# Kernel optimization log

Hardware: AMD Instinct MI355X
Metric: run time of the kernel (lower is better)

The kernel has to match this reference:

```python
import jax, jax.numpy as jnp
import numpy as np

SEQ_LEN = 4096
D_IN = 1024
D_OUT = 1024


def setup_inputs() -> dict:
    key = jax.random.key(0)
    k_x, k_q, k_k, k_v = jax.random.split(key, 4)
    s = 1.0 / np.sqrt(D_IN)
    return {
        "x": jax.random.normal(k_x, (SEQ_LEN, D_IN), dtype=jnp.float32),
        "W_query": jax.random.normal(k_q, (D_IN, D_OUT), dtype=jnp.float32) * s,
        "W_key": jax.random.normal(k_k, (D_IN, D_OUT), dtype=jnp.float32) * s,
        "W_value": jax.random.normal(k_v, (D_IN, D_OUT), dtype=jnp.float32) * s,
    }


def reference(x, W_query, W_key, W_value):
    # QKV projections (Linear without bias): [S, d_out]
    q = x @ W_query
    k = x @ W_key
    v = x @ W_value
    # Full S x S score matrix, causal mask, scaled softmax
    scores = q @ k.T  # [S, S]
    seq_len = x.shape[0]
    causal = jnp.tril(jnp.ones((seq_len, seq_len), dtype=bool))
    scores = jnp.where(causal, scores, -jnp.inf)
    scale = 1.0 / jnp.sqrt(jnp.asarray(k.shape[-1], dtype=scores.dtype))
    attn = jax.nn.softmax(scores * scale, axis=-1)
    return attn @ v  # [S, d_out]
```

## Files before the change

### kernel.cpp

```cpp
#include <hip/hip_runtime.h>
#include <math.h>

#define SEQ 4096
#define DIM 1024

typedef unsigned short u16;
typedef __attribute__((ext_vector_type(8))) short short8;
typedef __attribute__((ext_vector_type(4))) float floatx4;
typedef __attribute__((ext_vector_type(4))) unsigned short us4;

__device__ __forceinline__ float bf2f(u16 u) {
    union { unsigned int i; float f; } c; c.i = ((unsigned int)u) << 16; return c.f;
}
__device__ __forceinline__ u16 f2bf(float f) {
    union { float f; unsigned int i; } c; c.f = f;
    return (u16)((c.i + 0x7fffu + ((c.i >> 16) & 1u)) >> 16);
}
__device__ __forceinline__ void gload_lds16(const u16* g, u16* l) {
    __builtin_amdgcn_global_load_lds((const __attribute__((address_space(1))) void*)g,
                                     (__attribute__((address_space(3))) void*)l, 16, 0, 0);
}

template <int MODE>
__global__ __launch_bounds__(256) void gemm_nt(const u16* __restrict__ A,
                                               const u16* __restrict__ B,
                                               void* __restrict__ Cv,
                                               u16* __restrict__ VtOut,
                                               float* __restrict__ Lsum,
                                               int lda, int ldb, int ldc, int Kdim,
                                               float scale0) {
    int row0, col0, kbeg = 0, kend = Kdim;
    if (MODE == 1) {
        const int t = blockIdx.x;
        int by = (int)((sqrtf(8.0f * t + 1.0f) - 1.0f) * 0.5f);
        while ((by + 1) * (by + 2) / 2 <= t) ++by;
        while (by * (by + 1) / 2 > t) --by;
        const int bx = t - by * (by + 1) / 2;
        row0 = by * 128;
        col0 = bx * 128;
    } else if (MODE == 2) {
        col0 = blockIdx.x * 128;
        const int u = blockIdx.y;
        int r;
        if (u < 16) { r = 16 + u; kbeg = 0; kend = 2048; }
        else {
            r = 47 - u;
            kend = r * 128 + 128;
            kbeg = (u < 32) ? 2048 : 0;
        }
        row0 = r * 128;
    } else {
        row0 = blockIdx.y * 128;
        col0 = blockIdx.x * 128;
    }

    __shared__ u16 As[3][4096];
    __shared__ u16 Bs[3][4096];

    const int tid  = threadIdx.x;
    const int wave = tid >> 6;
    const int lane = tid & 63;
    const int wm = wave & 1;
    const int wn = wave >> 1;

    const int s0 = wave * 128 + lane;
    const int s1 = s0 + 64;
    const int r0s = s0 >> 2, q0s = ((s0 & 3) ^ ((s0 >> 3) & 3)) * 8;
    const int r1s = s1 >> 2, q1s = ((s1 & 3) ^ ((s1 >> 3) & 3)) * 8;
    const u16* aP0 = A + (size_t)(row0 + r0s) * lda + kbeg + q0s;
    const u16* aP1 = A + (size_t)(row0 + r1s) * lda + kbeg + q1s;
    const u16* bP0 = B + (size_t)(col0 + r0s) * ldb + kbeg + q0s;
    const u16* bP1 = B + (size_t)(col0 + r1s) * ldb + kbeg + q1s;
    const int l0 = wave * 1024;

    floatx4 acc[4][4] = {};
    const int niter = (kend - kbeg) >> 5;
    const int frow = lane & 15;
    const int xq = (((lane >> 4) ^ ((frow >> 1) & 3))) * 8;

    gload_lds16(aP0, &As[0][l0]);
    gload_lds16(aP1, &As[0][l0 + 512]);
    gload_lds16(bP0, &Bs[0][l0]);
    gload_lds16(bP1, &Bs[0][l0 + 512]);
    aP0 += 32; aP1 += 32; bP0 += 32; bP1 += 32;
    gload_lds16(aP0, &As[1][l0]);
    gload_lds16(aP1, &As[1][l0 + 512]);
    gload_lds16(bP0, &Bs[1][l0]);
    gload_lds16(bP1, &Bs[1][l0 + 512]);
    aP0 += 32; aP1 += 32; bP0 += 32; bP1 += 32;

    auto compute_tile = [&](int c) {
        short8 af[4], bfr[4];
#pragma unroll
        for (int t = 0; t < 4; ++t) {
            af[t]  = *(const short8*)&As[c][(wm * 64 + t * 16 + frow) * 32 + xq];
            bfr[t] = *(const short8*)&Bs[c][(wn * 64 + t * 16 + frow) * 32 + xq];
        }
#pragma unroll
        for (int mt = 0; mt < 4; ++mt)
#pragma unroll
            for (int nt = 0; nt < 4; ++nt)
                acc[mt][nt] = __builtin_amdgcn_mfma_f32_16x16x32_bf16(
                    af[mt], bfr[nt], acc[mt][nt], 0, 0, 0);
    };

    int cur = 0, pre = 2;
    for (int it = 0; it < niter - 2; ++it) {
        asm volatile("s_waitcnt vmcnt(4)\n\ts_barrier" ::: "memory");
        short8 af[4], bfr[4];
#pragma unroll
        for (int t = 0; t < 4; ++t) {
            af[t]  = *(const short8*)&As[cur][(wm * 64 + t * 16 + frow) * 32 + xq];
            bfr[t] = *(const short8*)&Bs[cur][(wn * 64 + t * 16 + frow) * 32 + xq];
        }
        gload_lds16(aP0, &As[pre][l0]);
        gload_lds16(aP1, &As[pre][l0 + 512]);
        gload_lds16(bP0, &Bs[pre][l0]);
        gload_lds16(bP1, &Bs[pre][l0 + 512]);
        aP0 += 32; aP1 += 32; bP0 += 32; bP1 += 32;
#pragma unroll
        for (int mt = 0; mt < 4; ++mt)
#pragma unroll
            for (int nt = 0; nt < 4; ++nt)
                acc[mt][nt] = __builtin_amdgcn_mfma_f32_16x16x32_bf16(
                    af[mt], bfr[nt], acc[mt][nt], 0, 0, 0);
        cur = (cur == 2) ? 0 : cur + 1;
        pre = (pre == 2) ? 0 : pre + 1;
    }
    asm volatile("s_waitcnt vmcnt(4)\n\ts_barrier" ::: "memory");
    compute_tile(cur);
    cur = (cur == 2) ? 0 : cur + 1;
    asm volatile("s_waitcnt vmcnt(0)\n\ts_barrier" ::: "memory");
    compute_tile(cur);

    const int cr = (lane >> 4) * 4;
    const int cc = lane & 15;
    if (MODE == 1) {
        u16* dst = (u16*)Cv;
#pragma unroll
        for (int mt = 0; mt < 4; ++mt) {
#pragma unroll
            for (int r = 0; r < 4; ++r) {
                const int grow = row0 + wm * 64 + mt * 16 + cr + r;
                float rowsum = 0.f;
#pragma unroll
                for (int nt = 0; nt < 4; ++nt) {
                    const int gcol = col0 + wn * 64 + nt * 16 + cc;
                    const float e = (gcol <= grow) ? __expf(acc[mt][nt][r]) : 0.f;
                    rowsum += e;
                    dst[(size_t)grow * ldc + gcol] = f2bf(e);
                }
                rowsum += __shfl_xor(rowsum, 1);
                rowsum += __shfl_xor(rowsum, 2);
                rowsum += __shfl_xor(rowsum, 4);
                rowsum += __shfl_xor(rowsum, 8);
                if (cc == 0) atomicAdd(&Lsum[grow], rowsum);
            }
        }
    } else if (MODE == 2) {
        float* O = (float*)Cv;
        const bool direct = (kbeg == 0) && (kend == row0 + 128);
#pragma unroll
        for (int mt = 0; mt < 4; ++mt)
#pragma unroll
            for (int r = 0; r < 4; ++r) {
                const int grow = row0 + wm * 64 + mt * 16 + cr + r;
                const float invl = __builtin_amdgcn_rcpf(Lsum[grow]);
#pragma unroll
                for (int nt = 0; nt < 4; ++nt) {
                    const int col = col0 + wn * 64 + nt * 16 + cc;
                    const float v = acc[mt][nt][r] * invl;
                    if (direct)
                        O[(size_t)grow * ldc + col] = v;
                    else
                        atomicAdd(&O[(size_t)grow * ldc + col], v);
                }
            }
    } else if (MODE == 0 && col0 >= 2048) {
#pragma unroll
        for (int mt = 0; mt < 4; ++mt)
#pragma unroll
            for (int nt = 0; nt < 4; ++nt) {
                const int row = row0 + wm * 64 + mt * 16 + cr;
                const int col = (col0 - 2048) + wn * 64 + nt * 16 + cc;
                us4 o = { f2bf(acc[mt][nt][0]), f2bf(acc[mt][nt][1]),
                          f2bf(acc[mt][nt][2]), f2bf(acc[mt][nt][3]) };
                *(us4*)&VtOut[(size_t)col * SEQ + row] = o;
            }
    } else {
        u16* dst = (u16*)Cv;
        const float sc = (col0 < 1024) ? scale0 : 1.0f;
#pragma unroll
        for (int mt = 0; mt < 4; ++mt)
#pragma unroll
            for (int nt = 0; nt < 4; ++nt)
#pragma unroll
                for (int r = 0; r < 4; ++r) {
                    const int row = row0 + wm * 64 + mt * 16 + cr + r;
                    const int col = col0 + wn * 64 + nt * 16 + cc;
                    dst[(size_t)row * ldc + col] = f2bf(acc[mt][nt][r] * sc);
                }
    }
}

__global__ __launch_bounds__(256) void prep(const float* __restrict__ x,
                                            const float* __restrict__ W0,
                                            const float* __restrict__ W1,
                                            const float* __restrict__ W2,
                                            u16* __restrict__ xb,
                                            u16* __restrict__ Wt,
                                            float* __restrict__ O,
                                            float* __restrict__ Lsum) {
    __shared__ float tile[32][33];
    const int b = blockIdx.x;
    const int tid = threadIdx.x;
    if (b < 4096) {
        const size_t i = ((size_t)b * 256 + tid) * 4;
        const float4 v = *(const float4*)(x + i);
        us4 o = { f2bf(v.x), f2bf(v.y), f2bf(v.z), f2bf(v.w) };
        *(us4*)(xb + i) = o;
    } else if (b < 7168) {
        const int t = b - 4096;
        const int z = t >> 10;
        const int idx = t & 1023;
        const float* W = (z == 0) ? W0 : (z == 1) ? W1 : W2;
        u16* out = Wt + (size_t)z * DIM * DIM;
        const int bx = (idx & 31) * 32;
        const int by = (idx >> 5) * 32;
        const int tx = tid & 31;
        const int ty = (tid >> 5) * 4;
#pragma unroll
        for (int r = 0; r < 4; ++r)
            tile[ty + r][tx] = W[(size_t)(by + ty + r) * DIM + bx + tx];
        __syncthreads();
#pragma unroll
        for (int r = 0; r < 4; ++r)
            out[(size_t)(bx + ty + r) * DIM + by + tx] = f2bf(tile[tx][ty + r]);
    } else {
        const int t = b - 7168;
        const size_t i = (size_t)2048 * DIM + ((size_t)t * 256 + tid) * 4;
        *(float4*)(O + i) = make_float4(0.f, 0.f, 0.f, 0.f);
        if (t < 4) *(float4*)(Lsum + (size_t)(t * 256 + tid) * 4) =
            make_float4(0.f, 0.f, 0.f, 0.f);
    }
}

extern "C" void kernel_launch(void* const* d_in, const int* in_sizes, int n_in,
                              void* d_out, int out_size, void* d_ws, size_t ws_size,
                              hipStream_t stream) {
    const float* x  = (const float*)d_in[0];
    const float* Wq = (const float*)d_in[1];
    const float* Wk = (const float*)d_in[2];
    const float* Wv = (const float*)d_in[3];

    u16* xb    = (u16*)d_ws;
    u16* Wt    = xb  + (size_t)SEQ * DIM;
    u16* QK    = Wt  + (size_t)3072 * DIM;
    u16* Vt    = QK  + (size_t)SEQ * 2048;
    u16* E     = Vt  + (size_t)DIM * SEQ;
    float* Lsum = (float*)(E + (size_t)SEQ * SEQ);

    prep<<<7680, 256, 0, stream>>>(x, Wq, Wk, Wv, xb, Wt, (float*)d_out, Lsum);

    gemm_nt<0><<<dim3(24, 32), 256, 0, stream>>>(
        xb, Wt, QK, Vt, nullptr, DIM, DIM, 2048, DIM, 0.03125f);

    gemm_nt<1><<<528, 256, 0, stream>>>(
        QK, QK + 1024, E, nullptr, Lsum, 2048, 2048, SEQ, DIM, 1.0f);

    gemm_nt<2><<<dim3(8, 48), 256, 0, stream>>>(
        E, Vt, d_out, nullptr, Lsum, SEQ, SEQ, DIM, SEQ, 1.0f);
}
```

Before: 191.5 us.

## Use 64-row tiles in PV GEMM with paired scheduling, drop split-K atomics

The attention-times-V GEMM now uses 64x128 output tiles over 512 blocks, pairing short and long causal rows by interleaving, so each block covers its full K range. This replaces the earlier 128-row tiling with split-K and float atomicAdd, and removes the zero-initialisation of the output in the prep kernel. The cost is lower MFMA reuse per block (2x4 instead of 4x4 tiles) and more B-tile reloads, and the longest blocks now walk all 4096 K columns alone.

```diff
diff --git a/kernel.cpp b/kernel.cpp
--- a/kernel.cpp
+++ b/kernel.cpp
@@ -40,21 +40,17 @@
         col0 = bx * 128;
     } else if (MODE == 2) {
         col0 = blockIdx.x * 128;
-        const int u = blockIdx.y;
-        int r;
-        if (u < 16) { r = 16 + u; kbeg = 0; kend = 2048; }
-        else {
-            r = 47 - u;
-            kend = r * 128 + 128;
-            kbeg = (u < 32) ? 2048 : 0;
-        }
-        row0 = r * 128;
+        const int y = blockIdx.y;
+        const int r = (y < 32) ? (y << 1) : (63 - ((y - 32) << 1));
+        row0 = r * 64;
+        kbeg = 0;
+        kend = row0 + 64;
     } else {
         row0 = blockIdx.y * 128;
         col0 = blockIdx.x * 128;
     }
 
-    __shared__ u16 As[3][4096];
+    __shared__ u16 As[3][(MODE == 2) ? 2048 : 4096];
     __shared__ u16 Bs[3][4096];
 
     const int tid  = threadIdx.x;
@@ -63,41 +59,50 @@
     const int wm = wave & 1;
     const int wn = wave >> 1;
 
-    const int s0 = wave * 128 + lane;
-    const int s1 = s0 + 64;
-    const int r0s = s0 >> 2, q0s = ((s0 & 3) ^ ((s0 >> 3) & 3)) * 8;
-    const int r1s = s1 >> 2, q1s = ((s1 & 3) ^ ((s1 >> 3) & 3)) * 8;
-    const u16* aP0 = A + (size_t)(row0 + r0s) * lda + kbeg + q0s;
-    const u16* aP1 = A + (size_t)(row0 + r1s) * lda + kbeg + q1s;
-    const u16* bP0 = B + (size_t)(col0 + r0s) * ldb + kbeg + q0s;
-    const u16* bP1 = B + (size_t)(col0 + r1s) * ldb + kbeg + q1s;
-    const int l0 = wave * 1024;
-
-    floatx4 acc[4][4] = {};
+    const int sB0 = wave * 128 + lane;
+    const int sB1 = sB0 + 64;
+    const int rB0 = sB0 >> 2, qB0 = ((sB0 & 3) ^ ((sB0 >> 3) & 3)) * 8;
+    const int rB1 = sB1 >> 2, qB1 = ((sB1 & 3) ^ ((sB1 >> 3) & 3)) * 8;
+    const int sA0 = (MODE == 2) ? (wave * 64 + lane) : sB0;
+    const int rA0 = sA0 >> 2, qA0 = ((sA0 & 3) ^ ((sA0 >> 3) & 3)) * 8;
+
+    const u16* aP0 = A + (size_t)(row0 + rA0) * lda + kbeg + qA0;
+    const u16* aP1 = A + (size_t)(row0 + rB1) * lda + kbeg + qB1;
+    const u16* bP0 = B + (size_t)(col0 + rB0) * ldb + kbeg + qB0;
+    const u16* bP1 = B + (size_t)(col0 + rB1) * ldb + kbeg + qB1;
+    const int lA0 = (MODE == 2) ? wave * 512 : wave * 1024;
+    const int lB0 = wave * 1024;
+
+    constexpr int MT = (MODE == 2) ? 2 : 4;
+    floatx4 acc[MT][4] = {};
     const int niter = (kend - kbeg) >> 5;
     const int frow = lane & 15;
     const int xq = (((lane >> 4) ^ ((frow >> 1) & 3))) * 8;
-
-    gload_lds16(aP0, &As[0][l0]);
-    gload_lds16(aP1, &As[0][l0 + 512]);
-    gload_lds16(bP0, &Bs[0][l0]);
-    gload_lds16(bP1, &Bs[0][l0 + 512]);
-    aP0 += 32; aP1 += 32; bP0 += 32; bP1 += 32;
-    gload_lds16(aP0, &As[1][l0]);
-    gload_lds16(aP1, &As[1][l0 + 512]);
-    gload_lds16(bP0, &Bs[1][l0]);
-    gload_lds16(bP1, &Bs[1][l0 + 512]);
-    aP0 += 32; aP1 += 32; bP0 += 32; bP1 += 32;
+    const int mrow0 = (MODE == 2) ? wm * 32 : wm * 64;
+
+    auto stage = [&](int c) {
+        gload_lds16(aP0, &As[c][lA0]);
+        if constexpr (MODE != 2) gload_lds16(aP1, &As[c][lA0 + 512]);
+        gload_lds16(bP0, &Bs[c][lB0]);
+        gload_lds16(bP1, &Bs[c][lB0 + 512]);
+        aP0 += 32;
+        if constexpr (MODE != 2) aP1 += 32;
+        bP0 += 32; bP1 += 32;
+    };
+
+    stage(0);
+    stage(1);
 
     auto compute_tile = [&](int c) {
-        short8 af[4], bfr[4];
-#pragma unroll
-        for (int t = 0; t < 4; ++t) {
-            af[t]  = *(const short8*)&As[c][(wm * 64 + t * 16 + frow) * 32 + xq];
+        short8 af[MT], bfr[4];
+#pragma unroll
+        for (int t = 0; t < MT; ++t)
+            af[t] = *(const short8*)&As[c][(mrow0 + t * 16 + frow) * 32 + xq];
+#pragma unroll
+        for (int t = 0; t < 4; ++t)
             bfr[t] = *(const short8*)&Bs[c][(wn * 64 + t * 16 + frow) * 32 + xq];
-        }
-#pragma unroll
-        for (int mt = 0; mt < 4; ++mt)
+#pragma unroll
+        for (int mt = 0; mt < MT; ++mt)
 #pragma unroll
             for (int nt = 0; nt < 4; ++nt)
                 acc[mt][nt] = __builtin_amdgcn_mfma_f32_16x16x32_bf16(
@@ -106,20 +111,20 @@
 
     int cur = 0, pre = 2;
     for (int it = 0; it < niter - 2; ++it) {
-        asm volatile("s_waitcnt vmcnt(4)\n\ts_barrier" ::: "memory");
-        short8 af[4], bfr[4];
-#pragma unroll
-        for (int t = 0; t < 4; ++t) {
-            af[t]  = *(const short8*)&As[cur][(wm * 64 + t * 16 + frow) * 32 + xq];
+        if constexpr (MODE == 2)
+            asm volatile("s_waitcnt vmcnt(3)\n\ts_barrier" ::: "memory");
+        else
+            asm volatile("s_waitcnt vmcnt(4)\n\ts_barrier" ::: "memory");
+        short8 af[MT], bfr[4];
+#pragma unroll
+        for (int t = 0; t < MT; ++t)
+            af[t] = *(const short8*)&As[cur][(mrow0 + t * 16 + frow) * 32 + xq];
+#pragma unroll
+        for (int t = 0; t < 4; ++t)
             bfr[t] = *(const short8*)&Bs[cur][(wn * 64 + t * 16 + frow) * 32 + xq];
-        }
-        gload_lds16(aP0, &As[pre][l0]);
-        gload_lds16(aP1, &As[pre][l0 + 512]);
-        gload_lds16(bP0, &Bs[pre][l0]);
-        gload_lds16(bP1, &Bs[pre][l0 + 512]);
-        aP0 += 32; aP1 += 32; bP0 += 32; bP1 += 32;
-#pragma unroll
-        for (int mt = 0; mt < 4; ++mt)
+        stage(pre);
+#pragma unroll
+        for (int mt = 0; mt < MT; ++mt)
 #pragma unroll
             for (int nt = 0; nt < 4; ++nt)
                 acc[mt][nt] = __builtin_amdgcn_mfma_f32_16x16x32_bf16(
@@ -127,7 +132,10 @@
         cur = (cur == 2) ? 0 : cur + 1;
         pre = (pre == 2) ? 0 : pre + 1;
     }
-    asm volatile("s_waitcnt vmcnt(4)\n\ts_barrier" ::: "memory");
+    if constexpr (MODE == 2)
+        asm volatile("s_waitcnt vmcnt(3)\n\ts_barrier" ::: "memory");
+    else
+        asm volatile("s_waitcnt vmcnt(4)\n\ts_barrier" ::: "memory");
     compute_tile(cur);
     cur = (cur == 2) ? 0 : cur + 1;
     asm volatile("s_waitcnt vmcnt(0)\n\ts_barrier" ::: "memory");
@@ -138,7 +146,7 @@
     if (MODE == 1) {
         u16* dst = (u16*)Cv;
 #pragma unroll
-        for (int mt = 0; mt < 4; ++mt) {
+        for (int mt = 0; mt < MT; ++mt) {
 #pragma unroll
             for (int r = 0; r < 4; ++r) {
                 const int grow = row0 + wm * 64 + mt * 16 + cr + r;
@@ -159,26 +167,21 @@
         }
     } else if (MODE == 2) {
         float* O = (float*)Cv;
-        const bool direct = (kbeg == 0) && (kend == row0 + 128);
-#pragma unroll
-        for (int mt = 0; mt < 4; ++mt)
+#pragma unroll
+        for (int mt = 0; mt < MT; ++mt)
 #pragma unroll
             for (int r = 0; r < 4; ++r) {
-                const int grow = row0 + wm * 64 + mt * 16 + cr + r;
+                const int grow = row0 + wm * 32 + mt * 16 + cr + r;
                 const float invl = __builtin_amdgcn_rcpf(Lsum[grow]);
 #pragma unroll
                 for (int nt = 0; nt < 4; ++nt) {
                     const int col = col0 + wn * 64 + nt * 16 + cc;
-                    const float v = acc[mt][nt][r] * invl;
-                    if (direct)
-                        O[(size_t)grow * ldc + col] = v;
-                    else
-                        atomicAdd(&O[(size_t)grow * ldc + col], v);
+                    O[(size_t)grow * ldc + col] = acc[mt][nt][r] * invl;
                 }
             }
     } else if (MODE == 0 && col0 >= 2048) {
 #pragma unroll
-        for (int mt = 0; mt < 4; ++mt)
+        for (int mt = 0; mt < MT; ++mt)
 #pragma unroll
             for (int nt = 0; nt < 4; ++nt) {
                 const int row = row0 + wm * 64 + mt * 16 + cr;
@@ -191,7 +194,7 @@
         u16* dst = (u16*)Cv;
         const float sc = (col0 < 1024) ? scale0 : 1.0f;
 #pragma unroll
-        for (int mt = 0; mt < 4; ++mt)
+        for (int mt = 0; mt < MT; ++mt)
 #pragma unroll
             for (int nt = 0; nt < 4; ++nt)
 #pragma unroll
@@ -209,7 +212,6 @@
                                             const float* __restrict__ W2,
                                             u16* __restrict__ xb,
                                             u16* __restrict__ Wt,
-                                            float* __restrict__ O,
                                             float* __restrict__ Lsum) {
     __shared__ float tile[32][33];
     const int b = blockIdx.x;
@@ -238,9 +240,7 @@
             out[(size_t)(bx + ty + r) * DIM + by + tx] = f2bf(tile[tx][ty + r]);
     } else {
         const int t = b - 7168;
-        const size_t i = (size_t)2048 * DIM + ((size_t)t * 256 + tid) * 4;
-        *(float4*)(O + i) = make_float4(0.f, 0.f, 0.f, 0.f);
-        if (t < 4) *(float4*)(Lsum + (size_t)(t * 256 + tid) * 4) =
+        *(float4*)(Lsum + (size_t)(t * 256 + tid) * 4) =
             make_float4(0.f, 0.f, 0.f, 0.f);
     }
 }
@@ -260,7 +260,7 @@
     u16* E     = Vt  + (size_t)DIM * SEQ;
     float* Lsum = (float*)(E + (size_t)SEQ * SEQ);
 
-    prep<<<7680, 256, 0, stream>>>(x, Wq, Wk, Wv, xb, Wt, (float*)d_out, Lsum);
+    prep<<<7172, 256, 0, stream>>>(x, Wq, Wk, Wv, xb, Wt, Lsum);
 
     gemm_nt<0><<<dim3(24, 32), 256, 0, stream>>>(
         xb, Wt, QK, Vt, nullptr, DIM, DIM, 2048, DIM, 0.03125f);
@@ -268,6 +268,6 @@
     gemm_nt<1><<<528, 256, 0, stream>>>(
         QK, QK + 1024, E, nullptr, Lsum, 2048, 2048, SEQ, DIM, 1.0f);
 
-    gemm_nt<2><<<dim3(8, 48), 256, 0, stream>>>(
+    gemm_nt<2><<<dim3(8, 64), 256, 0, stream>>>(
         E, Vt, d_out, nullptr, Lsum, SEQ, SEQ, DIM, SEQ, 1.0f);
 }
```

Measured after the change: 189.1 us. No clear change (-1.3%).

## Use 64x64 tiles for scores and PV with dynamic longest-first scheduling

Applied to the files above, without the earlier changes.

The scores and PV stages drop the 128x128 triangular tiling and switch to 64x64 tiles. Scores uses 2080 lower-triangular tiles, so work above the diagonal shrinks. PV replaces split-K with atomics with a persistent kernel that pulls row-tiles from an atomic ticket counter, longest rows first, and writes the output directly without atomics or zeroing. Smaller tiles improve load balance and cut masked work, but each tile reuses less data and runs fewer MFMAs per LDS load.

```diff
diff --git a/kernel.cpp b/kernel.cpp
--- a/kernel.cpp
+++ b/kernel.cpp
@@ -21,38 +21,77 @@
                                      (__attribute__((address_space(3))) void*)l, 16, 0, 0);
 }
 
-template <int MODE>
-__global__ __launch_bounds__(256) void gemm_nt(const u16* __restrict__ A,
+__device__ __forceinline__ void tile64(const u16* __restrict__ A,
+                                       const u16* __restrict__ B,
+                                       u16 (&As)[3][2048], u16 (&Bs)[3][2048],
+                                       int lda, int ldb,
+                                       int row0, int col0, int kend,
+                                       int wave, int lane,
+                                       floatx4 (&acc)[2][2]) {
+    const int wm = wave & 1, wn = wave >> 1;
+    const int s0 = wave * 64 + lane;
+    const int r0 = s0 >> 2, q0 = ((s0 & 3) ^ ((s0 >> 3) & 3)) * 8;
+    const u16* aP = A + (size_t)(row0 + r0) * lda + q0;
+    const u16* bP = B + (size_t)(col0 + r0) * ldb + q0;
+    const int l0 = wave * 512;
+    const int frow = lane & 15;
+    const int xq = (((lane >> 4) ^ ((frow >> 1) & 3))) * 8;
+    const int mrow0 = wm * 32, nrow0 = wn * 32;
+    const int niter = kend >> 5;
+
+    gload_lds16(aP, &As[0][l0]); gload_lds16(bP, &Bs[0][l0]); aP += 32; bP += 32;
+    gload_lds16(aP, &As[1][l0]); gload_lds16(bP, &Bs[1][l0]); aP += 32; bP += 32;
+
+    int cur = 0, pre = 2;
+    for (int it = 0; it < niter - 2; ++it) {
+        asm volatile("s_waitcnt vmcnt(2)\n\ts_barrier" ::: "memory");
+        short8 af[2], bfr[2];
+#pragma unroll
+        for (int t = 0; t < 2; ++t) {
+            af[t]  = *(const short8*)&As[cur][(mrow0 + t * 16 + frow) * 32 + xq];
+            bfr[t] = *(const short8*)&Bs[cur][(nrow0 + t * 16 + frow) * 32 + xq];
+        }
+        gload_lds16(aP, &As[pre][l0]); gload_lds16(bP, &Bs[pre][l0]);
+        aP += 32; bP += 32;
+#pragma unroll
+        for (int mt = 0; mt < 2; ++mt)
+#pragma unroll
+            for (int nt = 0; nt < 2; ++nt)
+                acc[mt][nt] = __builtin_amdgcn_mfma_f32_16x16x32_bf16(
+                    af[mt], bfr[nt], acc[mt][nt], 0, 0, 0);
+        cur = (cur == 2) ? 0 : cur + 1;
+        pre = (pre == 2) ? 0 : pre + 1;
+    }
+#pragma unroll
+    for (int fin = 0; fin < 2; ++fin) {
+        if (fin == 0)
+            asm volatile("s_waitcnt vmcnt(2)\n\ts_barrier" ::: "memory");
+        else
+            asm volatile("s_waitcnt vmcnt(0)\n\ts_barrier" ::: "memory");
+        short8 af[2], bfr[2];
+#pragma unroll
+        for (int t = 0; t < 2; ++t) {
+            af[t]  = *(const short8*)&As[cur][(mrow0 + t * 16 + frow) * 32 + xq];
+            bfr[t] = *(const short8*)&Bs[cur][(nrow0 + t * 16 + frow) * 32 + xq];
+        }
+#pragma unroll
+        for (int mt = 0; mt < 2; ++mt)
+#pragma unroll
+            for (int nt = 0; nt < 2; ++nt)
+                acc[mt][nt] = __builtin_amdgcn_mfma_f32_16x16x32_bf16(
+                    af[mt], bfr[nt], acc[mt][nt], 0, 0, 0);
+        cur = (cur == 2) ? 0 : cur + 1;
+    }
+}
+
+__global__ __launch_bounds__(256) void gemm128(const u16* __restrict__ A,
                                                const u16* __restrict__ B,
-                                               void* __restrict__ Cv,
+                                               u16* __restrict__ Cout,
                                                u16* __restrict__ VtOut,
-                                               float* __restrict__ Lsum,
                                                int lda, int ldb, int ldc, int Kdim,
                                                float scale0) {
-    int row0, col0, kbeg = 0, kend = Kdim;
-    if (MODE == 1) {
-        const int t = blockIdx.x;
-        int by = (int)((sqrtf(8.0f * t + 1.0f) - 1.0f) * 0.5f);
-        while ((by + 1) * (by + 2) / 2 <= t) ++by;
-        while (by * (by + 1) / 2 > t) --by;
-        const int bx = t - by * (by + 1) / 2;
-        row0 = by * 128;
-        col0 = bx * 128;
-    } else if (MODE == 2) {
-        col0 = blockIdx.x * 128;
-        const int u = blockIdx.y;
-        int r;
-        if (u < 16) { r = 16 + u; kbeg = 0; kend = 2048; }
-        else {
-            r = 47 - u;
-            kend = r * 128 + 128;
-            kbeg = (u < 32) ? 2048 : 0;
-        }
-        row0 = r * 128;
-    } else {
-        row0 = blockIdx.y * 128;
-        col0 = blockIdx.x * 128;
-    }
+    const int row0 = blockIdx.y * 128;
+    const int col0 = blockIdx.x * 128;
 
     __shared__ u16 As[3][4096];
     __shared__ u16 Bs[3][4096];
@@ -67,27 +106,26 @@
     const int s1 = s0 + 64;
     const int r0s = s0 >> 2, q0s = ((s0 & 3) ^ ((s0 >> 3) & 3)) * 8;
     const int r1s = s1 >> 2, q1s = ((s1 & 3) ^ ((s1 >> 3) & 3)) * 8;
-    const u16* aP0 = A + (size_t)(row0 + r0s) * lda + kbeg + q0s;
-    const u16* aP1 = A + (size_t)(row0 + r1s) * lda + kbeg + q1s;
-    const u16* bP0 = B + (size_t)(col0 + r0s) * ldb + kbeg + q0s;
-    const u16* bP1 = B + (size_t)(col0 + r1s) * ldb + kbeg + q1s;
+    const u16* aP0 = A + (size_t)(row0 + r0s) * lda + q0s;
+    const u16* aP1 = A + (size_t)(row0 + r1s) * lda + q1s;
+    const u16* bP0 = B + (size_t)(col0 + r0s) * ldb + q0s;
+    const u16* bP1 = B + (size_t)(col0 + r1s) * ldb + q1s;
     const int l0 = wave * 1024;
 
     floatx4 acc[4][4] = {};
-    const int niter = (kend - kbeg) >> 5;
+    const int niter = Kdim >> 5;
     const int frow = lane & 15;
     const int xq = (((lane >> 4) ^ ((frow >> 1) & 3))) * 8;
 
-    gload_lds16(aP0, &As[0][l0]);
-    gload_lds16(aP1, &As[0][l0 + 512]);
-    gload_lds16(bP0, &Bs[0][l0]);
-    gload_lds16(bP1, &Bs[0][l0 + 512]);
-    aP0 += 32; aP1 += 32; bP0 += 32; bP1 += 32;
-    gload_lds16(aP0, &As[1][l0]);
-    gload_lds16(aP1, &As[1][l0 + 512]);
-    gload_lds16(bP0, &Bs[1][l0]);
-    gload_lds16(bP1, &Bs[1][l0 + 512]);
-    aP0 += 32; aP1 += 32; bP0 += 32; bP1 += 32;
+    auto stage = [&](int c) {
+        gload_lds16(aP0, &As[c][l0]);
+        gload_lds16(aP1, &As[c][l0 + 512]);
+        gload_lds16(bP0, &Bs[c][l0]);
+        gload_lds16(bP1, &Bs[c][l0 + 512]);
+        aP0 += 32; aP1 += 32; bP0 += 32; bP1 += 32;
+    };
+    stage(0);
+    stage(1);
 
     auto compute_tile = [&](int c) {
         short8 af[4], bfr[4];
@@ -113,11 +151,7 @@
             af[t]  = *(const short8*)&As[cur][(wm * 64 + t * 16 + frow) * 32 + xq];
             bfr[t] = *(const short8*)&Bs[cur][(wn * 64 + t * 16 + frow) * 32 + xq];
         }
-        gload_lds16(aP0, &As[pre][l0]);
-        gload_lds16(aP1, &As[pre][l0 + 512]);
-        gload_lds16(bP0, &Bs[pre][l0]);
-        gload_lds16(bP1, &Bs[pre][l0 + 512]);
-        aP0 += 32; aP1 += 32; bP0 += 32; bP1 += 32;
+        stage(pre);
 #pragma unroll
         for (int mt = 0; mt < 4; ++mt)
 #pragma unroll
@@ -135,48 +169,7 @@
 
     const int cr = (lane >> 4) * 4;
     const int cc = lane & 15;
-    if (MODE == 1) {
-        u16* dst = (u16*)Cv;
-#pragma unroll
-        for (int mt = 0; mt < 4; ++mt) {
-#pragma unroll
-            for (int r = 0; r < 4; ++r) {
-                const int grow = row0 + wm * 64 + mt * 16 + cr + r;
-                float rowsum = 0.f;
-#pragma unroll
-                for (int nt = 0; nt < 4; ++nt) {
-                    const int gcol = col0 + wn * 64 + nt * 16 + cc;
-                    const float e = (gcol <= grow) ? __expf(acc[mt][nt][r]) : 0.f;
-                    rowsum += e;
-                    dst[(size_t)grow * ldc + gcol] = f2bf(e);
-                }
-                rowsum += __shfl_xor(rowsum, 1);
-                rowsum += __shfl_xor(rowsum, 2);
-                rowsum += __shfl_xor(rowsum, 4);
-                rowsum += __shfl_xor(rowsum, 8);
-                if (cc == 0) atomicAdd(&Lsum[grow], rowsum);
-            }
-        }
-    } else if (MODE == 2) {
-        float* O = (float*)Cv;
-        const bool direct = (kbeg == 0) && (kend == row0 + 128);
-#pragma unroll
-        for (int mt = 0; mt < 4; ++mt)
-#pragma unroll
-            for (int r = 0; r < 4; ++r) {
-                const int grow = row0 + wm * 64 + mt * 16 + cr + r;
-                const float invl = __builtin_amdgcn_rcpf(Lsum[grow]);
-#pragma unroll
-                for (int nt = 0; nt < 4; ++nt) {
-                    const int col = col0 + wn * 64 + nt * 16 + cc;
-                    const float v = acc[mt][nt][r] * invl;
-                    if (direct)
-                        O[(size_t)grow * ldc + col] = v;
-                    else
-                        atomicAdd(&O[(size_t)grow * ldc + col], v);
-                }
-            }
-    } else if (MODE == 0 && col0 >= 2048) {
+    if (col0 >= 2048) {
 #pragma unroll
         for (int mt = 0; mt < 4; ++mt)
 #pragma unroll
@@ -188,7 +181,6 @@
                 *(us4*)&VtOut[(size_t)col * SEQ + row] = o;
             }
     } else {
-        u16* dst = (u16*)Cv;
         const float sc = (col0 < 1024) ? scale0 : 1.0f;
 #pragma unroll
         for (int mt = 0; mt < 4; ++mt)
@@ -198,8 +190,86 @@
                 for (int r = 0; r < 4; ++r) {
                     const int row = row0 + wm * 64 + mt * 16 + cr + r;
                     const int col = col0 + wn * 64 + nt * 16 + cc;
-                    dst[(size_t)row * ldc + col] = f2bf(acc[mt][nt][r] * sc);
+                    Cout[(size_t)row * ldc + col] = f2bf(acc[mt][nt][r] * sc);
                 }
+    }
+}
+
+__global__ __launch_bounds__(256) void scores64(const u16* __restrict__ QK,
+                                                u16* __restrict__ E,
+                                                float* __restrict__ Lsum) {
+    const int t = blockIdx.x;
+    int by = (int)((sqrtf(8.0f * t + 1.0f) - 1.0f) * 0.5f);
+    while ((by + 1) * (by + 2) / 2 <= t) ++by;
+    while (by * (by + 1) / 2 > t) --by;
+    const int bx = t - by * (by + 1) / 2;
+    const int row0 = by * 64, col0 = bx * 64;
+
+    __shared__ u16 As[3][2048], Bs[3][2048];
+    const int tid = threadIdx.x, wave = tid >> 6, lane = tid & 63;
+
+    floatx4 acc[2][2] = {};
+    tile64(QK, QK + 1024, As, Bs, 2048, 2048, row0, col0, DIM, wave, lane, acc);
+
+    const int wm = wave & 1, wn = wave >> 1;
+    const int cr = (lane >> 4) * 4, cc = lane & 15;
+#pragma unroll
+    for (int mt = 0; mt < 2; ++mt) {
+#pragma unroll
+        for (int r = 0; r < 4; ++r) {
+            const int grow = row0 + wm * 32 + mt * 16 + cr + r;
+            float rowsum = 0.f;
+#pragma unroll
+            for (int nt = 0; nt < 2; ++nt) {
+                const int gcol = col0 + wn * 32 + nt * 16 + cc;
+                const float e = (gcol <= grow) ? __expf(acc[mt][nt][r]) : 0.f;
+                rowsum += e;
+                E[(size_t)grow * SEQ + gcol] = f2bf(e);
+            }
+            rowsum += __shfl_xor(rowsum, 1);
+            rowsum += __shfl_xor(rowsum, 2);
+            rowsum += __shfl_xor(rowsum, 4);
+            rowsum += __shfl_xor(rowsum, 8);
+            if (cc == 0) atomicAdd(&Lsum[grow], rowsum);
+        }
+    }
+}
+
+__global__ __launch_bounds__(256) void pv64(const u16* __restrict__ E,
+                                            const u16* __restrict__ Vt,
+                                            float* __restrict__ O,
+                                            const float* __restrict__ Lsum,
+                                            unsigned* __restrict__ Tick) {
+    __shared__ u16 As[3][2048], Bs[3][2048];
+    __shared__ unsigned sh_t;
+    const int tid = threadIdx.x, wave = tid >> 6, lane = tid & 63;
+    const int wm = wave & 1, wn = wave >> 1;
+    const int cr = (lane >> 4) * 4, cc = lane & 15;
+
+    for (;;) {
+        if (tid == 0) sh_t = atomicAdd(Tick, 1u);
+        __syncthreads();
+        const unsigned t = sh_t;
+        if (t >= 1024u) return;
+        const int r = 63 - (int)(t >> 4);
+        const int x = (int)(t & 15u);
+        const int row0 = r * 64, col0 = x * 64;
+
+        floatx4 acc[2][2] = {};
+        tile64(E, Vt, As, Bs, SEQ, SEQ, row0, col0, row0 + 64, wave, lane, acc);
+
+#pragma unroll
+        for (int mt = 0; mt < 2; ++mt)
+#pragma unroll
+            for (int rr = 0; rr < 4; ++rr) {
+                const int grow = row0 + wm * 32 + mt * 16 + cr + rr;
+                const float invl = __builtin_amdgcn_rcpf(Lsum[grow]);
+#pragma unroll
+                for (int nt = 0; nt < 2; ++nt) {
+                    const int col = col0 + wn * 32 + nt * 16 + cc;
+                    O[(size_t)grow * DIM + col] = acc[mt][nt][rr] * invl;
+                }
+            }
     }
 }
 
@@ -209,8 +279,8 @@
                                             const float* __restrict__ W2,
                                             u16* __restrict__ xb,
                                             u16* __restrict__ Wt,
-                                            float* __restrict__ O,
-                                            float* __restrict__ Lsum) {
+                                            float* __restrict__ Lsum,
+                                            unsigned* __restrict__ Tick) {
     __shared__ float tile[32][33];
     const int b = blockIdx.x;
     const int tid = threadIdx.x;
@@ -238,10 +308,9 @@
             out[(size_t)(bx + ty + r) * DIM + by + tx] = f2bf(tile[tx][ty + r]);
     } else {
         const int t = b - 7168;
-        const size_t i = (size_t)2048 * DIM + ((size_t)t * 256 + tid) * 4;
-        *(float4*)(O + i) = make_float4(0.f, 0.f, 0.f, 0.f);
-        if (t < 4) *(float4*)(Lsum + (size_t)(t * 256 + tid) * 4) =
+        *(float4*)(Lsum + (size_t)(t * 256 + tid) * 4) =
             make_float4(0.f, 0.f, 0.f, 0.f);
+        if (t == 0 && tid == 0) *Tick = 0u;
     }
 }
 
@@ -259,15 +328,14 @@
     u16* Vt    = QK  + (size_t)SEQ * 2048;
     u16* E     = Vt  + (size_t)DIM * SEQ;
     float* Lsum = (float*)(E + (size_t)SEQ * SEQ);
-
-    prep<<<7680, 256, 0, stream>>>(x, Wq, Wk, Wv, xb, Wt, (float*)d_out, Lsum);
-
-    gemm_nt<0><<<dim3(24, 32), 256, 0, stream>>>(
-        xb, Wt, QK, Vt, nullptr, DIM, DIM, 2048, DIM, 0.03125f);
-
-    gemm_nt<1><<<528, 256, 0, stream>>>(
-        QK, QK + 1024, E, nullptr, Lsum, 2048, 2048, SEQ, DIM, 1.0f);
-
-    gemm_nt<2><<<dim3(8, 48), 256, 0, stream>>>(
-        E, Vt, d_out, nullptr, Lsum, SEQ, SEQ, DIM, SEQ, 1.0f);
-}
+    unsigned* Tick = (unsigned*)(Lsum + SEQ);
+
+    prep<<<7172, 256, 0, stream>>>(x, Wq, Wk, Wv, xb, Wt, Lsum, Tick);
+
+    gemm128<<<dim3(24, 32), 256, 0, stream>>>(
+        xb, Wt, QK, Vt, DIM, DIM, 2048, DIM, 0.03125f);
+
+    scores64<<<2080, 256, 0, stream>>>(QK, E, Lsum);
+
+    pv64<<<768, 256, 0, stream>>>(E, Vt, (float*)d_out, Lsum, Tick);
+}
```

Result: slower. 220.9 us (+15.3%).
